# Optimization experiments

Measured on AMD Instinct MI355X. Metric: run time of the kernel, lower is better.

## Reference

```python
import jax, jax.numpy as jnp
import numpy as np

E, D, H, T = 8, 1024, 4096, 8192  # num_expert, d_model, d_hidden, total_tokens


def setup_inputs() -> dict:
    key = jax.random.key(0)
    k1, k2, k3, k4, k5 = jax.random.split(key, 5)
    inp = jax.random.normal(k1, (T, D), dtype=jnp.float32)
    # FMoELinear weights: [E, out_features, in_features], bias [E, out_features]
    w1 = jax.random.normal(k2, (E, H, D), dtype=jnp.float32) * 0.02
    b1 = jax.random.normal(k3, (E, H), dtype=jnp.float32) * 0.02
    w2 = jax.random.normal(k4, (E, D, H), dtype=jnp.float32) * 0.02
    b2 = jax.random.normal(k5, (E, D), dtype=jnp.float32) * 0.02
    # tokens are contiguous per expert; equal split here (counts may vary in general)
    fwd_expert_count = jnp.full((E,), T // E, dtype=jnp.int32)
    return {"inp": inp, "w1": w1, "b1": b1, "w2": w2, "b2": b2,
            "fwd_expert_count": fwd_expert_count}


def _expert_ids(counts, n_tokens):
    # token t belongs to expert e iff cumsum(counts)[e-1] <= t < cumsum(counts)[e]
    offsets = jnp.cumsum(counts)  # [E]
    t = jnp.arange(n_tokens)
    return jnp.sum(t[:, None] >= offsets[None, :], axis=1)  # [T] in [0, E]


def _grouped_linear(x, W, b, eid):
    # grouped GEMM: y[t] = W[eid[t]] @ x[t] + b[eid[t]]; tokens with eid >= E -> 0
    n_exp = W.shape[0]
    acc = jnp.zeros((x.shape[0], W.shape[1]), dtype=x.dtype)
    for e in range(n_exp):  # small fixed loop over experts
        ye = x @ W[e].T + b[e]
        acc = acc + jnp.where((eid == e)[:, None], ye, jnp.zeros((), x.dtype))
    return acc


def reference(inp, w1, b1, w2, b2, fwd_expert_count):
    eid = _expert_ids(fwd_expert_count, inp.shape[0])
    h = _grouped_linear(inp, w1, b1, eid)   # [T, H]
    h = jax.nn.gelu(h)
    out = _grouped_linear(h, w2, b2, eid)   # [T, D]
    return out
```

## Files before the change

kernel.cpp:

```cpp
#include <hip/hip_runtime.h>
#include <hip/hip_bf16.h>
#include <cstdint>
#include <cstddef>


using bf16 = __hip_bfloat16;
typedef __attribute__((ext_vector_type(8))) short bf16x8;
typedef __attribute__((ext_vector_type(4))) float f32x4;

#define BM 128
#define BN 128
#define BK 32

__device__ __forceinline__ float gelu_f(float x) {
  const float c0 = 0.7978845608028654f;
  const float c1 = 0.044715f;
  float u = c0 * (x + c1 * x * x * x);
  float t = 1.0f - 2.0f / (__expf(2.0f * u) + 1.0f);
  return 0.5f * x * (1.0f + t);
}

__device__ __forceinline__ void stage_f32(const float* g, bf16* lds,
                                          int srow, int seg, int ldg) {
#pragma unroll
  for (int h = 0; h < 2; ++h) {
    const float* p = g + (size_t)(srow + h * 64) * ldg + seg;
    f32x4 lo = *(const f32x4*)(p);
    f32x4 hi = *(const f32x4*)(p + 4);
    bf16 cv[8];
#pragma unroll
    for (int i = 0; i < 4; ++i) {
      cv[i]     = __float2bfloat16(lo[i]);
      cv[i + 4] = __float2bfloat16(hi[i]);
    }
    *(bf16x8*)&lds[(srow + h * 64) * BK + seg] = *(const bf16x8*)cv;
  }
}

__device__ __forceinline__ void stage_bf16(const bf16* g, bf16* lds,
                                           int srow, int seg, int ldg) {
#pragma unroll
  for (int h = 0; h < 2; ++h) {
    const bf16* p = g + (size_t)(srow + h * 64) * ldg + seg;
    *(bf16x8*)&lds[(srow + h * 64) * BK + seg] = *(const bf16x8*)p;
  }
}

template <bool AF32>
__global__ __launch_bounds__(256) void grouped_gemm_bt(
    const void* __restrict__ Av,
    const float* __restrict__ B,
    const float* __restrict__ bias,
    void* __restrict__ Cv,
    const int* __restrict__ counts,
    int E, int N, int K, int c_is_bf16_gelu)
{
  __shared__ alignas(16) bf16 As[BM * BK];
  __shared__ alignas(16) bf16 Bs[BN * BK];

  const int tid  = threadIdx.x;
  const int lane = tid & 63;
  const int wave = tid >> 6;
  const int m0 = blockIdx.y * BM;
  const int n0 = blockIdx.x * BN;

  int eid = 0;
  {
    long long cum = 0;
    for (int e = 0; e < E; ++e) { cum += counts[e]; if (m0 >= cum) eid = e + 1; }
  }

  const int wrow = (wave >> 1) * 64;
  const int wcol = (wave & 1) * 64;

  f32x4 acc[4][4] = {};

  if (eid < E) {
    const float* Bexp = B + (size_t)eid * (size_t)N * (size_t)K;
    const int srow = tid >> 2;
    const int seg  = (tid & 3) * 8;

    const int frow = lane & 15;
    const int fk   = (lane >> 4) * 8;

    for (int kt = 0; kt < K; kt += BK) {
      if (AF32)
        stage_f32((const float*)Av + (size_t)(m0 + srow) * K + kt - (size_t)srow * K,
                  As, srow, seg, K);
      else
        stage_bf16((const bf16*)Av + (size_t)(m0 + srow) * K + kt - (size_t)srow * K,
                   As, srow, seg, K);
      stage_f32(Bexp + (size_t)(n0 + srow) * K + kt - (size_t)srow * K,
                Bs, srow, seg, K);
      __syncthreads();

      bf16x8 af[4], bfr[4];
#pragma unroll
      for (int i = 0; i < 4; ++i)
        af[i] = *(const bf16x8*)&As[(wrow + i * 16 + frow) * BK + fk];
#pragma unroll
      for (int j = 0; j < 4; ++j)
        bfr[j] = *(const bf16x8*)&Bs[(wcol + j * 16 + frow) * BK + fk];

#pragma unroll
      for (int i = 0; i < 4; ++i)
#pragma unroll
        for (int j = 0; j < 4; ++j)
          acc[i][j] = __builtin_amdgcn_mfma_f32_16x16x32_bf16(af[i], bfr[j], acc[i][j], 0, 0, 0);

      __syncthreads();
    }
  }

  const int crow = (lane >> 4) * 4;
  const int ccol = lane & 15;
  const int do_gelu = c_is_bf16_gelu;

  if (eid < E) {
    float bv[4];
#pragma unroll
    for (int j = 0; j < 4; ++j)
      bv[j] = bias[(size_t)eid * N + n0 + wcol + j * 16 + ccol];
#pragma unroll
    for (int i = 0; i < 4; ++i) {
#pragma unroll
      for (int r = 0; r < 4; ++r) {
        size_t grow = (size_t)(m0 + wrow + i * 16 + crow + r);
#pragma unroll
        for (int j = 0; j < 4; ++j) {
          float v = acc[i][j][r] + bv[j];
          size_t idx = grow * N + n0 + wcol + j * 16 + ccol;
          if (do_gelu) ((bf16*)Cv)[idx] = __float2bfloat16(gelu_f(v));
          else         ((float*)Cv)[idx] = v;
        }
      }
    }
  } else {
#pragma unroll
    for (int i = 0; i < 4; ++i) {
#pragma unroll
      for (int r = 0; r < 4; ++r) {
        size_t grow = (size_t)(m0 + wrow + i * 16 + crow + r);
#pragma unroll
        for (int j = 0; j < 4; ++j) {
          size_t idx = grow * N + n0 + wcol + j * 16 + ccol;
          if (do_gelu) ((bf16*)Cv)[idx] = __float2bfloat16(0.0f);
          else         ((float*)Cv)[idx] = 0.0f;
        }
      }
    }
  }
}

extern "C" void kernel_launch(void* const* d_in, const int* in_sizes, int n_in,
                              void* d_out, int out_size, void* d_ws, size_t ws_size,
                              hipStream_t stream) {
  const float* inp = (const float*)d_in[0];
  const float* w1  = (const float*)d_in[1];
  const float* b1  = (const float*)d_in[2];
  const float* w2  = (const float*)d_in[3];
  const float* b2  = (const float*)d_in[4];
  const int* cnt   = (const int*)d_in[5];
  float* out = (float*)d_out;

  const int E = in_sizes[5];
  const int H = in_sizes[2] / E;
  const int D = in_sizes[4] / E;
  const int T = in_sizes[0] / D;

  bf16* h = (bf16*)d_ws;

  dim3 blk(256);
  dim3 g1(H / BN, T / BM);
  grouped_gemm_bt<true><<<g1, blk, 0, stream>>>(inp, w1, b1, h, cnt, E, H, D, 1);
  dim3 g2(D / BN, T / BM);
  grouped_gemm_bt<false><<<g2, blk, 0, stream>>>(h, w2, b2, out, cnt, E, D, H, 0);
}
```

Measured before the change: 553.3 us.

## Pre-convert inputs and weights to bf16 and stage tiles with async global-to-LDS loads

Adds separate kernels that convert the activations and each weight tensor from fp32 to bf16 in workspace. A new GEMM kernel then loads bf16 tiles straight into LDS with global_load_lds, replacing the in-kernel fp32 load, convert and LDS store. The aim is to cut repeated fp32 weight reads and conversion work inside the GEMM loop. The cost is extra conversion passes over the 128MB weight tensors plus more workspace, and the new path only runs when the workspace is large enough.

```diff
diff --git a/kernel.cpp b/kernel.cpp
--- a/kernel.cpp
+++ b/kernel.cpp
@@ -11,6 +11,13 @@
 #define BM 128
 #define BN 128
 #define BK 32
+
+typedef const __attribute__((address_space(1))) unsigned int g_u32;
+typedef __attribute__((address_space(3))) unsigned int l_u32;
+
+__device__ __forceinline__ void async16(void* lds, const void* g) {
+  __builtin_amdgcn_global_load_lds((g_u32*)g, (l_u32*)lds, 16, 0, 0);
+}
 
 __device__ __forceinline__ float gelu_f(float x) {
   const float c0 = 0.7978845608028654f;
@@ -20,36 +27,26 @@
   return 0.5f * x * (1.0f + t);
 }
 
-__device__ __forceinline__ void stage_f32(const float* g, bf16* lds,
-                                          int srow, int seg, int ldg) {
-#pragma unroll
-  for (int h = 0; h < 2; ++h) {
-    const float* p = g + (size_t)(srow + h * 64) * ldg + seg;
-    f32x4 lo = *(const f32x4*)(p);
-    f32x4 hi = *(const f32x4*)(p + 4);
+__global__ __launch_bounds__(256) void f32_to_bf16(
+    const float* __restrict__ in, bf16* __restrict__ out, size_t n) {
+  size_t i = ((size_t)blockIdx.x * blockDim.x + threadIdx.x) * 8;
+  const size_t stride = (size_t)gridDim.x * blockDim.x * 8;
+  for (; i < n; i += stride) {
+    f32x4 lo = *(const f32x4*)(in + i);
+    f32x4 hi = *(const f32x4*)(in + i + 4);
     bf16 cv[8];
 #pragma unroll
-    for (int i = 0; i < 4; ++i) {
-      cv[i]     = __float2bfloat16(lo[i]);
-      cv[i + 4] = __float2bfloat16(hi[i]);
-    }
-    *(bf16x8*)&lds[(srow + h * 64) * BK + seg] = *(const bf16x8*)cv;
-  }
-}
-
-__device__ __forceinline__ void stage_bf16(const bf16* g, bf16* lds,
-                                           int srow, int seg, int ldg) {
-#pragma unroll
-  for (int h = 0; h < 2; ++h) {
-    const bf16* p = g + (size_t)(srow + h * 64) * ldg + seg;
-    *(bf16x8*)&lds[(srow + h * 64) * BK + seg] = *(const bf16x8*)p;
-  }
-}
-
-template <bool AF32>
-__global__ __launch_bounds__(256) void grouped_gemm_bt(
-    const void* __restrict__ Av,
-    const float* __restrict__ B,
+    for (int k = 0; k < 4; ++k) {
+      cv[k]     = __float2bfloat16(lo[k]);
+      cv[k + 4] = __float2bfloat16(hi[k]);
+    }
+    *(bf16x8*)(out + i) = *(const bf16x8*)cv;
+  }
+}
+
+__global__ __launch_bounds__(256) void gemm_bt_bf16(
+    const bf16* __restrict__ A,
+    const bf16* __restrict__ B,
     const float* __restrict__ bias,
     void* __restrict__ Cv,
     const int* __restrict__ counts,
@@ -76,10 +73,140 @@
   f32x4 acc[4][4] = {};
 
   if (eid < E) {
+    const bf16* Bexp = B + (size_t)eid * (size_t)N * (size_t)K;
+
+    const int rA = lane >> 2;
+    const int sA = (lane & 3) * 8;
+
+    const int frow = lane & 15;
+    const int fk   = (lane >> 4) * 8;
+
+    for (int kt = 0; kt < K; kt += BK) {
+#pragma unroll
+      for (int c = 0; c < 2; ++c) {
+        const int chunk = wave * 2 + c;
+        const int row = chunk * 16 + rA;
+        async16(&As[chunk * 16 * BK],
+                A + (size_t)(m0 + row) * K + kt + sA);
+        async16(&Bs[chunk * 16 * BK],
+                Bexp + (size_t)(n0 + row) * K + kt + sA);
+      }
+      __syncthreads();
+
+      bf16x8 af[4], bfr[4];
+#pragma unroll
+      for (int i = 0; i < 4; ++i)
+        af[i] = *(const bf16x8*)&As[(wrow + i * 16 + frow) * BK + fk];
+#pragma unroll
+      for (int j = 0; j < 4; ++j)
+        bfr[j] = *(const bf16x8*)&Bs[(wcol + j * 16 + frow) * BK + fk];
+
+#pragma unroll
+      for (int i = 0; i < 4; ++i)
+#pragma unroll
+        for (int j = 0; j < 4; ++j)
+          acc[i][j] = __builtin_amdgcn_mfma_f32_16x16x32_bf16(af[i], bfr[j], acc[i][j], 0, 0, 0);
+
+      __syncthreads();
+    }
+  }
+
+  const int crow = (lane >> 4) * 4;
+  const int ccol = lane & 15;
+  const int do_gelu = c_is_bf16_gelu;
+
+  if (eid < E) {
+    float bv[4];
+#pragma unroll
+    for (int j = 0; j < 4; ++j)
+      bv[j] = bias[(size_t)eid * N + n0 + wcol + j * 16 + ccol];
+#pragma unroll
+    for (int i = 0; i < 4; ++i) {
+#pragma unroll
+      for (int r = 0; r < 4; ++r) {
+        size_t grow = (size_t)(m0 + wrow + i * 16 + crow + r);
+#pragma unroll
+        for (int j = 0; j < 4; ++j) {
+          float v = acc[i][j][r] + bv[j];
+          size_t idx = grow * N + n0 + wcol + j * 16 + ccol;
+          if (do_gelu) ((bf16*)Cv)[idx] = __float2bfloat16(gelu_f(v));
+          else         ((float*)Cv)[idx] = v;
+        }
+      }
+    }
+  } else {
+#pragma unroll
+    for (int i = 0; i < 4; ++i) {
+#pragma unroll
+      for (int r = 0; r < 4; ++r) {
+        size_t grow = (size_t)(m0 + wrow + i * 16 + crow + r);
+#pragma unroll
+        for (int j = 0; j < 4; ++j) {
+          size_t idx = grow * N + n0 + wcol + j * 16 + ccol;
+          if (do_gelu) ((bf16*)Cv)[idx] = __float2bfloat16(0.0f);
+          else         ((float*)Cv)[idx] = 0.0f;
+        }
+      }
+    }
+  }
+}
+
+__device__ __forceinline__ void stage_f32(const float* g, bf16* lds,
+                                          int srow, int seg, int ldg) {
+#pragma unroll
+  for (int h = 0; h < 2; ++h) {
+    const float* p = g + (size_t)(srow + h * 64) * ldg + seg;
+    f32x4 lo = *(const f32x4*)(p);
+    f32x4 hi = *(const f32x4*)(p + 4);
+    bf16 cv[8];
+#pragma unroll
+    for (int i = 0; i < 4; ++i) {
+      cv[i]     = __float2bfloat16(lo[i]);
+      cv[i + 4] = __float2bfloat16(hi[i]);
+    }
+    *(bf16x8*)&lds[(srow + h * 64) * BK + seg] = *(const bf16x8*)cv;
+  }
+}
+
+__device__ __forceinline__ void stage_bf16(const bf16* g, bf16* lds,
+                                           int srow, int seg, int ldg) {
+#pragma unroll
+  for (int h = 0; h < 2; ++h) {
+    const bf16* p = g + (size_t)(srow + h * 64) * ldg + seg;
+    *(bf16x8*)&lds[(srow + h * 64) * BK + seg] = *(const bf16x8*)p;
+  }
+}
+
+template <bool AF32>
+__global__ __launch_bounds__(256) void grouped_gemm_bt(
+    const void* __restrict__ Av, const float* __restrict__ B,
+    const float* __restrict__ bias, void* __restrict__ Cv,
+    const int* __restrict__ counts, int E, int N, int K, int c_is_bf16_gelu)
+{
+  __shared__ alignas(16) bf16 As[BM * BK];
+  __shared__ alignas(16) bf16 Bs[BN * BK];
+
+  const int tid  = threadIdx.x;
+  const int lane = tid & 63;
+  const int wave = tid >> 6;
+  const int m0 = blockIdx.y * BM;
+  const int n0 = blockIdx.x * BN;
+
+  int eid = 0;
+  {
+    long long cum = 0;
+    for (int e = 0; e < E; ++e) { cum += counts[e]; if (m0 >= cum) eid = e + 1; }
+  }
+
+  const int wrow = (wave >> 1) * 64;
+  const int wcol = (wave & 1) * 64;
+
+  f32x4 acc[4][4] = {};
+
+  if (eid < E) {
     const float* Bexp = B + (size_t)eid * (size_t)N * (size_t)K;
     const int srow = tid >> 2;
     const int seg  = (tid & 3) * 8;
-
     const int frow = lane & 15;
     const int fk   = (lane >> 4) * 8;
 
@@ -168,11 +295,28 @@
   const int D = in_sizes[4] / E;
   const int T = in_sizes[0] / D;
 
-  bf16* h = (bf16*)d_ws;
+  const size_t szH = (size_t)T * H * sizeof(bf16);
+  const size_t szX = (size_t)T * D * sizeof(bf16);
+  const size_t szW = (size_t)E * (size_t)H * D * sizeof(bf16);
 
   dim3 blk(256);
-  dim3 g1(H / BN, T / BM);
-  grouped_gemm_bt<true><<<g1, blk, 0, stream>>>(inp, w1, b1, h, cnt, E, H, D, 1);
-  dim3 g2(D / BN, T / BM);
-  grouped_gemm_bt<false><<<g2, blk, 0, stream>>>(h, w2, b2, out, cnt, E, D, H, 0);
-}
+
+  if (ws_size >= szH + szX + szW) {
+    bf16* h  = (bf16*)d_ws;
+    bf16* xb = (bf16*)((char*)d_ws + szH);
+    bf16* wb = (bf16*)((char*)d_ws + szH + szX);
+
+    const size_t nX = (size_t)T * D;
+    const size_t nW = (size_t)E * (size_t)H * D;
+
+    f32_to_bf16<<<dim3(1024), blk, 0, stream>>>(inp, xb, nX);
+    f32_to_bf16<<<dim3(2048), blk, 0, stream>>>(w1, wb, nW);
+    gemm_bt_bf16<<<dim3(H / BN, T / BM), blk, 0, stream>>>(xb, wb, b1, h, cnt, E, H, D, 1);
+    f32_to_bf16<<<dim3(2048), blk, 0, stream>>>(w2, wb, nW);
+    gemm_bt_bf16<<<dim3(D / BN, T / BM), blk, 0, stream>>>(h, wb, b2, out, cnt, E, D, H, 0);
+  } else {
+    bf16* h = (bf16*)d_ws;
+    grouped_gemm_bt<true><<<dim3(H / BN, T / BM), blk, 0, stream>>>(inp, w1, b1, h, cnt, E, H, D, 1);
+    grouped_gemm_bt<false><<<dim3(D / BN, T / BM), blk, 0, stream>>>(h, w2, b2, out, cnt, E, D, H, 0);
+  }
+}
```

After: 553.5 us. Within noise of the previous version (+0.0%).
